# Optimization experiments

Hardware: AMD Instinct MI355X
Metric: run time of the kernel (lower is better)

Reference implementation:

```python
import jax, jax.numpy as jnp
import numpy as np

N = 50000   # num_nodes
T = 24      # window_size
H = 64      # hidden_dim
HOR = 12    # horizon
E = 1600000 # num edges


def setup_inputs() -> dict:
    key = jax.random.key(0)
    ks = jax.random.split(key, 12)
    s = 1.0 / np.sqrt(H)
    u = lambda k, shape: jax.random.uniform(k, shape, jnp.float32, -s, s)
    return {
        "x": jax.random.normal(ks[0], (N, T), jnp.float32),
        "edge_index": jax.random.randint(ks[1], (2, E), 0, N, dtype=jnp.int32),
        "w_ih": u(ks[2], (3 * H, 1)),
        "w_hh": u(ks[3], (3 * H, H)),
        "b_ih": u(ks[4], (3 * H,)),
        "b_hh": u(ks[5], (3 * H,)),
        "gc1_w": u(ks[6], (H, H)),
        "gc1_b": u(ks[7], (H,)),
        "gc2_w": u(ks[8], (H, H)),
        "gc2_b": u(ks[9], (H,)),
        "fc_w": u(ks[10], (HOR, H)),
        "fc_b": u(ks[11], (HOR,)),
    }


def _gru_last(x, w_ih, w_hh, b_ih, b_hh):
    # x: [N, T] scalar-per-step input (input_size=1). Returns final hidden [N, H].
    h0 = jnp.zeros((x.shape[0], H), x.dtype)

    def step(h, xt):  # xt: [N]
        gi = xt[:, None] * w_ih[:, 0][None, :] + b_ih   # [N, 3H]
        gh = h @ w_hh.T + b_hh                          # [N, 3H]
        i_r, i_z, i_n = jnp.split(gi, 3, axis=-1)
        h_r, h_z, h_n = jnp.split(gh, 3, axis=-1)
        r = jax.nn.sigmoid(i_r + h_r)
        z = jax.nn.sigmoid(i_z + h_z)
        n = jnp.tanh(i_n + r * h_n)
        h = (1.0 - z) * n + z * h
        return h, None

    hT, _ = jax.lax.scan(step, h0, x.T)  # scan over time axis
    return hT


def _gcn_norm(edge_index, n):
    # PyG GCNConv: add self loops, symmetric D^-1/2 (A+I) D^-1/2 normalization.
    loops = jnp.arange(n, dtype=edge_index.dtype)
    src = jnp.concatenate([edge_index[0], loops])
    dst = jnp.concatenate([edge_index[1], loops])
    deg = jax.ops.segment_sum(jnp.ones(src.shape, jnp.float32), dst, num_segments=n)
    dinv = jnp.where(deg > 0, jax.lax.rsqrt(jnp.maximum(deg, 1e-12)), 0.0)
    return src, dst, dinv[src] * dinv[dst]


def _gcn(h, src, dst, norm, W, b, n):
    hw = h @ W.T                      # [N, H] linear transform first
    msg = hw[src] * norm[:, None]     # gather + edge weighting
    return jax.ops.segment_sum(msg, dst, num_segments=n) + b


def reference(x, edge_index, w_ih, w_hh, b_ih, b_hh, gc1_w, gc1_b, gc2_w, gc2_b, fc_w, fc_b):
    n = x.shape[0]
    h = _gru_last(x, w_ih, w_hh, b_ih, b_hh)            # [N, H] last GRU output
    src, dst, norm = _gcn_norm(edge_index, n)
    h = jax.nn.relu(_gcn(h, src, dst, norm, gc1_w, gc1_b, n))
    h = jax.nn.relu(_gcn(h, src, dst, norm, gc2_w, gc2_b, n))
    return h @ fc_w.T + fc_b                            # [N, HOR]
```

## Files before the change

kernel.cpp:

```cpp
#include <hip/hip_runtime.h>

#define NN 50000
#define TT 24
#define HH 64
#define HORZ 12
#define EE 1600000

#define GP 256
#define EP (EE / GP)
#define BK 784
#define NBG (BK * GP)
#define SCB (NBG / 512)
#define BKA ((NN + 63) / 64)

typedef __attribute__((ext_vector_type(8))) _Float16 f16x8;
typedef __attribute__((ext_vector_type(4))) _Float16 f16x4;
typedef __attribute__((ext_vector_type(4))) float f32x4;

__device__ __forceinline__ float sigm(float x) {
  return __builtin_amdgcn_rcpf(1.f + __expf(-x));
}
__device__ __forceinline__ float tanh_f(float x) {
  return 1.f - 2.f * __builtin_amdgcn_rcpf(1.f + __expf(2.f * x));
}

__global__ __launch_bounds__(256) void p1_frags_kernel(
    const int* __restrict__ dst, int* __restrict__ hist,
    const float* __restrict__ whh, const float* __restrict__ g1,
    const float* __restrict__ g2, const float* __restrict__ fcw,
    _Float16* __restrict__ frag) {
  int bid = blockIdx.x;
  if (bid >= GP) {
    int idx = (bid - GP) * 256 + threadIdx.x;
    if (idx >= 21504) return;
    const float* W;
    int rows, li;
    if (idx < 12288) { W = whh; rows = 192; li = idx; }
    else if (idx < 16384) { W = g1; rows = 64; li = idx - 12288; }
    else if (idx < 20480) { W = g2; rows = 64; li = idx - 16384; }
    else { W = fcw; rows = HORZ; li = idx - 20480; }
    int j = li & 7;
    int l = (li >> 3) & 63;
    int kf = (li >> 9) & 1;
    int nf = li >> 10;
    int col = 16 * nf + (l & 15);
    int k = 32 * kf + 8 * (l >> 4) + j;
    frag[idx] = (col < rows) ? (_Float16)W[col * 64 + k] : (_Float16)0.f;
    return;
  }
  __shared__ int h[BK];
  int tid = threadIdx.x, g = bid;
  for (int b = tid; b < BK; b += 256) h[b] = 0;
  __syncthreads();
  int e0 = g * EP;
  for (int i = tid; i < EP; i += 256) atomicAdd(&h[dst[e0 + i] >> 6], 1);
  __syncthreads();
  for (int b = tid; b < BK; b += 256) hist[b * GP + g] = h[b];
}

__global__ void scanA_kernel(const int* __restrict__ v, int* __restrict__ part) {
  __shared__ int s[512];
  int i = blockIdx.x * 512 + threadIdx.x;
  s[threadIdx.x] = v[i];
  __syncthreads();
  for (int off = 256; off > 0; off >>= 1) {
    if (threadIdx.x < off) s[threadIdx.x] += s[threadIdx.x + off];
    __syncthreads();
  }
  if (threadIdx.x == 0) part[blockIdx.x] = s[0];
}

__global__ void scanB_kernel(int* __restrict__ part) {
  __shared__ int s[512];
  int t = threadIdx.x;
  int v = (t < SCB) ? part[t] : 0;
  s[t] = v;
  __syncthreads();
  for (int off = 1; off < 512; off <<= 1) {
    int a = s[t];
    int b = (t >= off) ? s[t - off] : 0;
    __syncthreads();
    s[t] = a + b;
    __syncthreads();
  }
  if (t < SCB) part[t] = s[t] - v;
}

__global__ void scanC_kernel(int* __restrict__ cellbase, const int* __restrict__ part) {
  __shared__ int s[2][512];
  int tid = threadIdx.x;
  int i = blockIdx.x * 512 + tid;
  int x = cellbase[i];
  s[0][tid] = x;
  __syncthreads();
  int cur = 0;
  for (int off = 1; off < 512; off <<= 1) {
    int nxt = cur ^ 1;
    int val = s[cur][tid] + ((tid >= off) ? s[cur][tid - off] : 0);
    s[nxt][tid] = val;
    __syncthreads();
    cur = nxt;
  }
  cellbase[i] = part[blockIdx.x] + s[cur][tid] - x;
  if (i == 0) cellbase[NBG] = EE;
}

__global__ __launch_bounds__(256) void p2_scatter_kernel(
    const int* __restrict__ src, const int* __restrict__ dst,
    const int* __restrict__ cellbase, unsigned int* __restrict__ rec) {
  __shared__ int cur[BK];
  int tid = threadIdx.x, g = blockIdx.x;
  for (int b = tid; b < BK; b += 256) cur[b] = cellbase[b * GP + g];
  __syncthreads();
  int e0 = g * EP;
  for (int i = tid; i < EP; i += 256) {
    int e = e0 + i;
    int d = dst[e];
    int s = src[e];
    int p = atomicAdd(&cur[d >> 6], 1);
    rec[p] = ((unsigned)(d & 63) << 16) | (unsigned)s;
  }
}

__global__ __launch_bounds__(256) void sort2_kernel(
    const unsigned int* __restrict__ rec, const int* __restrict__ cellbase,
    unsigned short* __restrict__ csr, int* __restrict__ row_start,
    float* __restrict__ dinv) {
  __shared__ int cnt[64];
  __shared__ int cur[64];
  int b = blockIdx.x, tid = threadIdx.x;
  if (tid < 64) cnt[tid] = 0;
  __syncthreads();
  int e0 = cellbase[b * GP], e1 = cellbase[(b + 1) * GP];
  for (int e = e0 + tid; e < e1; e += 256) atomicAdd(&cnt[rec[e] >> 16], 1);
  __syncthreads();
  if (tid == 0) {
    int a = e0;
#pragma unroll
    for (int l = 0; l < 64; ++l) { int c = cnt[l]; cur[l] = a; a += c; }
  }
  __syncthreads();
  if (tid < 64) {
    int n = b * 64 + tid;
    if (n <= NN) row_start[n] = cur[tid];
    if (n < NN) dinv[n] = rsqrtf((float)(cnt[tid] + 1));
  }
  __syncthreads();
  for (int e = e0 + tid; e < e1; e += 256) {
    unsigned int r = rec[e];
    int p = atomicAdd(&cur[r >> 16], 1);
    csr[p] = (unsigned short)(r & 0xFFFFu);
  }
}

__global__ __launch_bounds__(256, 5) void gru_kernel(
    const float* __restrict__ x, const float* __restrict__ w_ih,
    const float* __restrict__ b_ih, const float* __restrict__ b_hh,
    const _Float16* __restrict__ wfrag, const _Float16* __restrict__ l1f,
    const float* __restrict__ dinv, _Float16* __restrict__ hw) {
  __shared__ __align__(16) _Float16 sh[2][16][72];
  __shared__ __align__(16) float xs[TT][16];

  const int tid = threadIdx.x;
  const int lane = tid & 63;
  const int w = tid >> 6;
  const int c = lane & 15;
  const int q = lane >> 4;

  f16x8 Ar0 = *(const f16x8*)&wfrag[(((w)*2 + 0) * 64 + lane) * 8];
  f16x8 Ar1 = *(const f16x8*)&wfrag[(((w)*2 + 1) * 64 + lane) * 8];
  f16x8 Az0 = *(const f16x8*)&wfrag[(((4 + w) * 2 + 0) * 64 + lane) * 8];
  f16x8 Az1 = *(const f16x8*)&wfrag[(((4 + w) * 2 + 1) * 64 + lane) * 8];
  f16x8 An0 = *(const f16x8*)&wfrag[(((8 + w) * 2 + 0) * 64 + lane) * 8];
  f16x8 An1 = *(const f16x8*)&wfrag[(((8 + w) * 2 + 1) * 64 + lane) * 8];

  float wir[4], wiz[4], win[4], arb[4], azb[4], binc[4], bhnc[4];
#pragma unroll
  for (int r = 0; r < 4; ++r) {
    int dd = 16 * w + 4 * q + r;
    wir[r] = w_ih[dd]; wiz[r] = w_ih[64 + dd]; win[r] = w_ih[128 + dd];
    arb[r] = b_ih[dd] + b_hh[dd];
    azb[r] = b_ih[64 + dd] + b_hh[64 + dd];
    binc[r] = b_ih[128 + dd];
    bhnc[r] = b_hh[128 + dd];
  }

  const int base = blockIdx.x * 16;

  for (int i = tid; i < 16 * TT; i += 256) {
    int nl = i / TT;
    int t = i - nl * TT;
    xs[t][nl] = x[(base + nl) * TT + t];
  }
  __syncthreads();

  float hreg[4] = {0.f, 0.f, 0.f, 0.f};

#pragma unroll 1
  for (int tp = 0; tp < TT / 2; ++tp) {
#pragma unroll
    for (int half = 0; half < 2; ++half) {
      const int t = 2 * tp + half;
      f32x4 ar = (f32x4){arb[0], arb[1], arb[2], arb[3]};
      f32x4 az = (f32x4){azb[0], azb[1], azb[2], azb[3]};
      f32x4 an = (f32x4){bhnc[0], bhnc[1], bhnc[2], bhnc[3]};
      if (t > 0) {
        const _Float16* S = &sh[half ^ 1][0][0];
        f16x8 b0 = *(const f16x8*)&S[c * 72 + 8 * q];
        f16x8 b1 = *(const f16x8*)&S[c * 72 + 32 + 8 * q];
        ar = __builtin_amdgcn_mfma_f32_16x16x32_f16(Ar0, b0, ar, 0, 0, 0);
        az = __builtin_amdgcn_mfma_f32_16x16x32_f16(Az0, b0, az, 0, 0, 0);
        an = __builtin_amdgcn_mfma_f32_16x16x32_f16(An0, b0, an, 0, 0, 0);
        ar = __builtin_amdgcn_mfma_f32_16x16x32_f16(Ar1, b1, ar, 0, 0, 0);
        az = __builtin_amdgcn_mfma_f32_16x16x32_f16(Az1, b1, az, 0, 0, 0);
        an = __builtin_amdgcn_mfma_f32_16x16x32_f16(An1, b1, an, 0, 0, 0);
      }
      float xv = xs[t][c];
      f16x4 hpack;
#pragma unroll
      for (int r = 0; r < 4; ++r) {
        float rg = sigm(xv * wir[r] + ar[r]);
        float zg = sigm(xv * wiz[r] + az[r]);
        float nn = tanh_f(rg * an[r] + (xv * win[r] + binc[r]));
        float hn = nn + zg * (hreg[r] - nn);
        hreg[r] = hn;
        hpack[r] = (_Float16)hn;
      }
      *(f16x4*)&sh[half][c][16 * w + 4 * q] = hpack;
      __syncthreads();
    }
  }

  {
    f16x8 L0 = *(const f16x8*)&l1f[((w * 2 + 0) * 64 + lane) * 8];
    f16x8 L1 = *(const f16x8*)&l1f[((w * 2 + 1) * 64 + lane) * 8];
    const _Float16* S = &sh[1][0][0];
    f16x8 b0 = *(const f16x8*)&S[c * 72 + 8 * q];
    f16x8 b1 = *(const f16x8*)&S[c * 72 + 32 + 8 * q];
    f32x4 acc = (f32x4){0.f, 0.f, 0.f, 0.f};
    acc = __builtin_amdgcn_mfma_f32_16x16x32_f16(L0, b0, acc, 0, 0, 0);
    acc = __builtin_amdgcn_mfma_f32_16x16x32_f16(L1, b1, acc, 0, 0, 0);
    float dn = dinv[base + c];
    f16x4 opack;
#pragma unroll
    for (int r = 0; r < 4; ++r) opack[r] = (_Float16)(acc[r] * dn);
    *(f16x4*)&hw[(base + c) * 64 + 16 * w + 4 * q] = opack;
  }
}

__global__ __launch_bounds__(1024, 4) void agg_lin_kernel(
    const _Float16* __restrict__ hwp, const float* __restrict__ dinv,
    const int* __restrict__ row_start, const unsigned short* __restrict__ csr,
    const float* __restrict__ bias, const _Float16* __restrict__ l2f,
    _Float16* __restrict__ out) {
  __shared__ __align__(16) _Float16 h1[64][72];
  int tid = threadIdx.x, b = blockIdx.x;
  int wv = tid >> 6, lane = tid & 63;
  float bl = bias[lane];
#pragma unroll 1
  for (int k = 0; k < 4; ++k) {
    int row = wv * 4 + k;
    int n = b * 64 + row;
    float v = 0.f;
    if (n < NN) {
      int e0 = row_start[n], e1 = row_start[n + 1];
      float a0 = (float)hwp[n * 64 + lane];
      float a1 = 0.f, a2 = 0.f, a3 = 0.f;
      int e = e0;
      for (; e < e1 && (e & 7); ++e) a0 += (float)hwp[(int)csr[e] * 64 + lane];
      for (; e + 16 <= e1; e += 16) {
        uint4 p0 = *(const uint4*)&csr[e];
        uint4 p1 = *(const uint4*)&csr[e + 8];
        a0 += (float)hwp[(p0.x & 0xFFFF) * 64 + lane];
        a1 += (float)hwp[(p0.x >> 16) * 64 + lane];
        a2 += (float)hwp[(p0.y & 0xFFFF) * 64 + lane];
        a3 += (float)hwp[(p0.y >> 16) * 64 + lane];
        a0 += (float)hwp[(p0.z & 0xFFFF) * 64 + lane];
        a1 += (float)hwp[(p0.z >> 16) * 64 + lane];
        a2 += (float)hwp[(p0.w & 0xFFFF) * 64 + lane];
        a3 += (float)hwp[(p0.w >> 16) * 64 + lane];
        a0 += (float)hwp[(p1.x & 0xFFFF) * 64 + lane];
        a1 += (float)hwp[(p1.x >> 16) * 64 + lane];
        a2 += (float)hwp[(p1.y & 0xFFFF) * 64 + lane];
        a3 += (float)hwp[(p1.y >> 16) * 64 + lane];
        a0 += (float)hwp[(p1.z & 0xFFFF) * 64 + lane];
        a1 += (float)hwp[(p1.z >> 16) * 64 + lane];
        a2 += (float)hwp[(p1.w & 0xFFFF) * 64 + lane];
        a3 += (float)hwp[(p1.w >> 16) * 64 + lane];
      }
      for (; e + 8 <= e1; e += 8) {
        uint4 pk = *(const uint4*)&csr[e];
        a0 += (float)hwp[(pk.x & 0xFFFF) * 64 + lane];
        a1 += (float)hwp[(pk.x >> 16) * 64 + lane];
        a2 += (float)hwp[(pk.y & 0xFFFF) * 64 + lane];
        a3 += (float)hwp[(pk.y >> 16) * 64 + lane];
        a0 += (float)hwp[(pk.z & 0xFFFF) * 64 + lane];
        a1 += (float)hwp[(pk.z >> 16) * 64 + lane];
        a2 += (float)hwp[(pk.w & 0xFFFF) * 64 + lane];
        a3 += (float)hwp[(pk.w >> 16) * 64 + lane];
      }
      for (; e < e1; ++e) a0 += (float)hwp[(int)csr[e] * 64 + lane];
      v = (a0 + a1 + a2 + a3) * dinv[n] + bl;
      v = v > 0.f ? v : 0.f;
    }
    h1[row][lane] = (_Float16)v;
  }
  __syncthreads();
  int g = wv >> 2, wq = wv & 3;
  int c = lane & 15, q = lane >> 4;
  f16x8 B0 = *(const f16x8*)&l2f[((wq * 2 + 0) * 64 + lane) * 8];
  f16x8 B1 = *(const f16x8*)&l2f[((wq * 2 + 1) * 64 + lane) * 8];
  f16x8 a0 = *(const f16x8*)&h1[16 * g + c][8 * q];
  f16x8 a1 = *(const f16x8*)&h1[16 * g + c][32 + 8 * q];
  f32x4 acc = (f32x4){0.f, 0.f, 0.f, 0.f};
  acc = __builtin_amdgcn_mfma_f32_16x16x32_f16(a0, B0, acc, 0, 0, 0);
  acc = __builtin_amdgcn_mfma_f32_16x16x32_f16(a1, B1, acc, 0, 0, 0);
#pragma unroll
  for (int r = 0; r < 4; ++r) {
    int n = b * 64 + 16 * g + 4 * q + r;
    if (n < NN) out[n * 64 + 16 * wq + c] = (_Float16)(acc[r] * dinv[n]);
  }
}

__global__ __launch_bounds__(1024, 4) void agg_fc_kernel(
    const _Float16* __restrict__ hwp, const float* __restrict__ dinv,
    const int* __restrict__ row_start, const unsigned short* __restrict__ csr,
    const float* __restrict__ bias, const _Float16* __restrict__ fcf,
    const float* __restrict__ fcb, float* __restrict__ out) {
  __shared__ __align__(16) _Float16 h1[64][72];
  int tid = threadIdx.x, b = blockIdx.x;
  int wv = tid >> 6, lane = tid & 63;
  float bl = bias[lane];
#pragma unroll 1
  for (int k = 0; k < 4; ++k) {
    int row = wv * 4 + k;
    int n = b * 64 + row;
    float v = 0.f;
    if (n < NN) {
      int e0 = row_start[n], e1 = row_start[n + 1];
      float a0 = (float)hwp[n * 64 + lane];
      float a1 = 0.f, a2 = 0.f, a3 = 0.f;
      int e = e0;
      for (; e < e1 && (e & 7); ++e) a0 += (float)hwp[(int)csr[e] * 64 + lane];
      for (; e + 16 <= e1; e += 16) {
        uint4 p0 = *(const uint4*)&csr[e];
        uint4 p1 = *(const uint4*)&csr[e + 8];
        a0 += (float)hwp[(p0.x & 0xFFFF) * 64 + lane];
        a1 += (float)hwp[(p0.x >> 16) * 64 + lane];
        a2 += (float)hwp[(p0.y & 0xFFFF) * 64 + lane];
        a3 += (float)hwp[(p0.y >> 16) * 64 + lane];
        a0 += (float)hwp[(p0.z & 0xFFFF) * 64 + lane];
        a1 += (float)hwp[(p0.z >> 16) * 64 + lane];
        a2 += (float)hwp[(p0.w & 0xFFFF) * 64 + lane];
        a3 += (float)hwp[(p0.w >> 16) * 64 + lane];
        a0 += (float)hwp[(p1.x & 0xFFFF) * 64 + lane];
        a1 += (float)hwp[(p1.x >> 16) * 64 + lane];
        a2 += (float)hwp[(p1.y & 0xFFFF) * 64 + lane];
        a3 += (float)hwp[(p1.y >> 16) * 64 + lane];
        a0 += (float)hwp[(p1.z & 0xFFFF) * 64 + lane];
        a1 += (float)hwp[(p1.z >> 16) * 64 + lane];
        a2 += (float)hwp[(p1.w & 0xFFFF) * 64 + lane];
        a3 += (float)hwp[(p1.w >> 16) * 64 + lane];
      }
      for (; e + 8 <= e1; e += 8) {
        uint4 pk = *(const uint4*)&csr[e];
        a0 += (float)hwp[(pk.x & 0xFFFF) * 64 + lane];
        a1 += (float)hwp[(pk.x >> 16) * 64 + lane];
        a2 += (float)hwp[(pk.y & 0xFFFF) * 64 + lane];
        a3 += (float)hwp[(pk.y >> 16) * 64 + lane];
        a0 += (float)hwp[(pk.z & 0xFFFF) * 64 + lane];
        a1 += (float)hwp[(pk.z >> 16) * 64 + lane];
        a2 += (float)hwp[(pk.w & 0xFFFF) * 64 + lane];
        a3 += (float)hwp[(pk.w >> 16) * 64 + lane];
      }
      for (; e < e1; ++e) a0 += (float)hwp[(int)csr[e] * 64 + lane];
      v = (a0 + a1 + a2 + a3) * dinv[n] + bl;
      v = v > 0.f ? v : 0.f;
    }
    h1[row][lane] = (_Float16)v;
  }
  __syncthreads();
  if (wv < 4) {
    int g = wv;
    int c = lane & 15, q = lane >> 4;
    f16x8 B0 = *(const f16x8*)&fcf[(0 * 64 + lane) * 8];
    f16x8 B1 = *(const f16x8*)&fcf[(1 * 64 + lane) * 8];
    f16x8 a0 = *(const f16x8*)&h1[16 * g + c][8 * q];
    f16x8 a1 = *(const f16x8*)&h1[16 * g + c][32 + 8 * q];
    float bc = (c < HORZ) ? fcb[c] : 0.f;
    f32x4 acc = (f32x4){bc, bc, bc, bc};
    acc = __builtin_amdgcn_mfma_f32_16x16x32_f16(a0, B0, acc, 0, 0, 0);
    acc = __builtin_amdgcn_mfma_f32_16x16x32_f16(a1, B1, acc, 0, 0, 0);
    if (c < HORZ) {
#pragma unroll
      for (int r = 0; r < 4; ++r) {
        int n = b * 64 + 16 * g + 4 * q + r;
        if (n < NN) out[n * HORZ + c] = acc[r];
      }
    }
  }
}

extern "C" void kernel_launch(void* const* d_in, const int* in_sizes, int n_in,
                              void* d_out, int out_size, void* d_ws, size_t ws_size,
                              hipStream_t stream) {
  (void)in_sizes; (void)n_in; (void)out_size; (void)ws_size;
  const float* x = (const float*)d_in[0];
  const int* edge_index = (const int*)d_in[1];
  const float* w_ih = (const float*)d_in[2];
  const float* w_hh = (const float*)d_in[3];
  const float* b_ih = (const float*)d_in[4];
  const float* b_hh = (const float*)d_in[5];
  const float* gc1_w = (const float*)d_in[6];
  const float* gc1_b = (const float*)d_in[7];
  const float* gc2_w = (const float*)d_in[8];
  const float* gc2_b = (const float*)d_in[9];
  const float* fc_w = (const float*)d_in[10];
  const float* fc_b = (const float*)d_in[11];
  float* out = (float*)d_out;

  char* ws = (char*)d_ws;
  _Float16* wfrag = (_Float16*)ws;
  _Float16* l1f = wfrag + 12288;
  _Float16* l2f = l1f + 4096;
  _Float16* fcf = l2f + 4096;
  _Float16* hw1 = (_Float16*)(ws + 43008);
  _Float16* hw2 = hw1 + NN * 64;
  float* dinv = (float*)(hw2 + NN * 64);
  int* row_start = (int*)(dinv + NN);
  int* cellbase = row_start + 50240;
  int* part = cellbase + NBG + 4;
  unsigned int* rec = (unsigned int*)(part + 512);
  unsigned short* csr = (unsigned short*)(rec + EE);

  const int* esrc = edge_index;
  const int* edst = edge_index + EE;

  p1_frags_kernel<<<GP + 84, 256, 0, stream>>>(edst, cellbase, w_hh, gc1_w, gc2_w, fc_w, wfrag);
  scanA_kernel<<<SCB, 512, 0, stream>>>(cellbase, part);
  scanB_kernel<<<1, 512, 0, stream>>>(part);
  scanC_kernel<<<SCB, 512, 0, stream>>>(cellbase, part);
  p2_scatter_kernel<<<GP, 256, 0, stream>>>(esrc, edst, cellbase, rec);
  sort2_kernel<<<BK, 256, 0, stream>>>(rec, cellbase, csr, row_start, dinv);

  gru_kernel<<<NN / 16, 256, 0, stream>>>(x, w_ih, b_ih, b_hh, wfrag, l1f, dinv, hw1);
  agg_lin_kernel<<<BKA, 1024, 0, stream>>>(hw1, dinv, row_start, csr, gc1_b, l2f, hw2);
  agg_fc_kernel<<<BKA, 1024, 0, stream>>>(hw2, dinv, row_start, csr, gc2_b, fcf, fc_b, out);
}
```

Before: 240.8 us.

## Give each GRU wave its own 16-node tile and fold input/bias into MFMA

The GRU kernel now gives each wave an independent 16-node tile and computes all 64 hidden units for it, so 64 nodes go to a block and the per-timestep block-wide __syncthreads is removed. The input term x*w_ih and the biases are folded into an extra MFMA against a fragment that holds x and 1, and the log2(e) scaling is baked into the fp16 weights so exp2f can be used. In exchange the kernel holds many more weight fragments in registers (launch bounds drop to 2), does more MFMA work per wave, and rounds the biases and input weights to fp16.

```diff
diff --git a/kernel.cpp b/kernel.cpp
--- a/kernel.cpp
+++ b/kernel.cpp
@@ -13,39 +13,66 @@
 #define SCB (NBG / 512)
 #define BKA ((NN + 63) / 64)
 
+#define L2E 1.44269504088896340736f
+#define NFRAG_GRU 24576
+#define NFRAG_ALL 33792
+
 typedef __attribute__((ext_vector_type(8))) _Float16 f16x8;
 typedef __attribute__((ext_vector_type(4))) _Float16 f16x4;
 typedef __attribute__((ext_vector_type(4))) float f32x4;
 
-__device__ __forceinline__ float sigm(float x) {
-  return __builtin_amdgcn_rcpf(1.f + __expf(-x));
-}
-__device__ __forceinline__ float tanh_f(float x) {
-  return 1.f - 2.f * __builtin_amdgcn_rcpf(1.f + __expf(2.f * x));
-}
-
 __global__ __launch_bounds__(256) void p1_frags_kernel(
     const int* __restrict__ dst, int* __restrict__ hist,
-    const float* __restrict__ whh, const float* __restrict__ g1,
-    const float* __restrict__ g2, const float* __restrict__ fcw,
-    _Float16* __restrict__ frag) {
+    const float* __restrict__ whh, const float* __restrict__ wih,
+    const float* __restrict__ bih, const float* __restrict__ bhh,
+    const float* __restrict__ g1, const float* __restrict__ g2,
+    const float* __restrict__ fcw, _Float16* __restrict__ frag) {
   int bid = blockIdx.x;
   if (bid >= GP) {
     int idx = (bid - GP) * 256 + threadIdx.x;
-    if (idx >= 21504) return;
-    const float* W;
-    int rows, li;
-    if (idx < 12288) { W = whh; rows = 192; li = idx; }
-    else if (idx < 16384) { W = g1; rows = 64; li = idx - 12288; }
-    else if (idx < 20480) { W = g2; rows = 64; li = idx - 16384; }
-    else { W = fcw; rows = HORZ; li = idx - 20480; }
-    int j = li & 7;
-    int l = (li >> 3) & 63;
-    int kf = (li >> 9) & 1;
-    int nf = li >> 10;
-    int col = 16 * nf + (l & 15);
-    int k = 32 * kf + 8 * (l >> 4) + j;
-    frag[idx] = (col < rows) ? (_Float16)W[col * 64 + k] : (_Float16)0.f;
+    if (idx >= NFRAG_ALL) return;
+    float v = 0.f;
+    if (idx < NFRAG_GRU) {
+      int tl = idx / 1536;
+      int rem = idx - tl * 1536;
+      int kf = rem >> 9;
+      int l = (rem >> 3) & 63;
+      int j = rem & 7;
+      int rit = l & 15;
+      int half = l >> 4;
+      if (tl < 12) {
+        int g = tl >> 2, dq = tl & 3;
+        int row = g * 64 + 16 * dq + rit;
+        float sc = (g == 2) ? 2.f * L2E : L2E;
+        if (kf < 2) {
+          v = whh[row * 64 + 32 * kf + 8 * half + j] * sc;
+        } else {
+          int kl = 8 * half + j;
+          if (kl == 0) v = (tl < 8) ? wih[row] * sc : 0.f;
+          else if (kl == 1) v = (tl < 8) ? (bih[row] + bhh[row]) * sc : bhh[row] * sc;
+        }
+      } else if (kf == 2) {
+        int row = 128 + 16 * (tl - 12) + rit;
+        int kl = 8 * half + j;
+        if (kl == 0) v = wih[row] * 2.f * L2E;
+        else if (kl == 1) v = bih[row] * 2.f * L2E;
+      }
+    } else {
+      int li = idx - NFRAG_GRU;
+      const float* W;
+      int rows;
+      if (li < 4096) { W = g1; rows = 64; }
+      else if (li < 8192) { W = g2; rows = 64; li -= 4096; }
+      else { W = fcw; rows = HORZ; li -= 8192; }
+      int j = li & 7;
+      int l = (li >> 3) & 63;
+      int kf = (li >> 9) & 1;
+      int nf = li >> 10;
+      int col = 16 * nf + (l & 15);
+      int k = 32 * kf + 8 * (l >> 4) + j;
+      v = (col < rows) ? W[col * 64 + k] : 0.f;
+    }
+    frag[idx] = (_Float16)v;
     return;
   }
   __shared__ int h[BK];
@@ -153,13 +180,12 @@
   }
 }
 
-__global__ __launch_bounds__(256, 5) void gru_kernel(
-    const float* __restrict__ x, const float* __restrict__ w_ih,
-    const float* __restrict__ b_ih, const float* __restrict__ b_hh,
-    const _Float16* __restrict__ wfrag, const _Float16* __restrict__ l1f,
-    const float* __restrict__ dinv, _Float16* __restrict__ hw) {
-  __shared__ __align__(16) _Float16 sh[2][16][72];
-  __shared__ __align__(16) float xs[TT][16];
+__global__ __launch_bounds__(256, 2) void gru_kernel(
+    const float* __restrict__ x, const _Float16* __restrict__ gf,
+    const _Float16* __restrict__ l1f, const float* __restrict__ dinv,
+    _Float16* __restrict__ hw) {
+  __shared__ __align__(16) _Float16 sh[4][2][16][72];
+  __shared__ __align__(16) float xs[TT][64];
 
   const int tid = threadIdx.x;
   const int lane = tid & 63;
@@ -167,84 +193,97 @@
   const int c = lane & 15;
   const int q = lane >> 4;
 
-  f16x8 Ar0 = *(const f16x8*)&wfrag[(((w)*2 + 0) * 64 + lane) * 8];
-  f16x8 Ar1 = *(const f16x8*)&wfrag[(((w)*2 + 1) * 64 + lane) * 8];
-  f16x8 Az0 = *(const f16x8*)&wfrag[(((4 + w) * 2 + 0) * 64 + lane) * 8];
-  f16x8 Az1 = *(const f16x8*)&wfrag[(((4 + w) * 2 + 1) * 64 + lane) * 8];
-  f16x8 An0 = *(const f16x8*)&wfrag[(((8 + w) * 2 + 0) * 64 + lane) * 8];
-  f16x8 An1 = *(const f16x8*)&wfrag[(((8 + w) * 2 + 1) * 64 + lane) * 8];
-
-  float wir[4], wiz[4], win[4], arb[4], azb[4], binc[4], bhnc[4];
-#pragma unroll
-  for (int r = 0; r < 4; ++r) {
-    int dd = 16 * w + 4 * q + r;
-    wir[r] = w_ih[dd]; wiz[r] = w_ih[64 + dd]; win[r] = w_ih[128 + dd];
-    arb[r] = b_ih[dd] + b_hh[dd];
-    azb[r] = b_ih[64 + dd] + b_hh[64 + dd];
-    binc[r] = b_ih[128 + dd];
-    bhnc[r] = b_hh[128 + dd];
-  }
-
-  const int base = blockIdx.x * 16;
-
-  for (int i = tid; i < 16 * TT; i += 256) {
+  f16x8 A0[12], A1[12], A2[16];
+#pragma unroll
+  for (int tl = 0; tl < 12; ++tl) {
+    A0[tl] = *(const f16x8*)&gf[((tl * 3 + 0) * 64 + lane) * 8];
+    A1[tl] = *(const f16x8*)&gf[((tl * 3 + 1) * 64 + lane) * 8];
+  }
+#pragma unroll
+  for (int tl = 0; tl < 16; ++tl)
+    A2[tl] = *(const f16x8*)&gf[((tl * 3 + 2) * 64 + lane) * 8];
+
+  const int nb = blockIdx.x * 64;
+  for (int i = tid; i < 64 * TT; i += 256) {
     int nl = i / TT;
     int t = i - nl * TT;
-    xs[t][nl] = x[(base + nl) * TT + t];
-  }
-  __syncthreads();
-
-  float hreg[4] = {0.f, 0.f, 0.f, 0.f};
+    int node = nb + nl;
+    if (node >= NN) node = NN - 1;
+    xs[t][nl] = x[node * TT + t];
+  }
+  {
+    f16x4 z4 = {(_Float16)0.f, (_Float16)0.f, (_Float16)0.f, (_Float16)0.f};
+#pragma unroll
+    for (int dq = 0; dq < 4; ++dq)
+      *(f16x4*)&sh[w][1][c][16 * dq + 4 * q] = z4;
+  }
+  __syncthreads();
+
+  const f32x4 zero4 = (f32x4){0.f, 0.f, 0.f, 0.f};
+  float hreg[4][4];
+#pragma unroll
+  for (int dq = 0; dq < 4; ++dq)
+#pragma unroll
+    for (int r = 0; r < 4; ++r) hreg[dq][r] = 0.f;
+
+  f16x8 b2 = {(_Float16)0.f, (_Float16)0.f, (_Float16)0.f, (_Float16)0.f,
+              (_Float16)0.f, (_Float16)0.f, (_Float16)0.f, (_Float16)0.f};
+  b2[1] = (q == 0) ? (_Float16)1.f : (_Float16)0.f;
 
 #pragma unroll 1
-  for (int tp = 0; tp < TT / 2; ++tp) {
-#pragma unroll
-    for (int half = 0; half < 2; ++half) {
-      const int t = 2 * tp + half;
-      f32x4 ar = (f32x4){arb[0], arb[1], arb[2], arb[3]};
-      f32x4 az = (f32x4){azb[0], azb[1], azb[2], azb[3]};
-      f32x4 an = (f32x4){bhnc[0], bhnc[1], bhnc[2], bhnc[3]};
-      if (t > 0) {
-        const _Float16* S = &sh[half ^ 1][0][0];
-        f16x8 b0 = *(const f16x8*)&S[c * 72 + 8 * q];
-        f16x8 b1 = *(const f16x8*)&S[c * 72 + 32 + 8 * q];
-        ar = __builtin_amdgcn_mfma_f32_16x16x32_f16(Ar0, b0, ar, 0, 0, 0);
-        az = __builtin_amdgcn_mfma_f32_16x16x32_f16(Az0, b0, az, 0, 0, 0);
-        an = __builtin_amdgcn_mfma_f32_16x16x32_f16(An0, b0, an, 0, 0, 0);
-        ar = __builtin_amdgcn_mfma_f32_16x16x32_f16(Ar1, b1, ar, 0, 0, 0);
-        az = __builtin_amdgcn_mfma_f32_16x16x32_f16(Az1, b1, az, 0, 0, 0);
-        an = __builtin_amdgcn_mfma_f32_16x16x32_f16(An1, b1, an, 0, 0, 0);
-      }
-      float xv = xs[t][c];
-      f16x4 hpack;
-#pragma unroll
-      for (int r = 0; r < 4; ++r) {
-        float rg = sigm(xv * wir[r] + ar[r]);
-        float zg = sigm(xv * wiz[r] + az[r]);
-        float nn = tanh_f(rg * an[r] + (xv * win[r] + binc[r]));
-        float hn = nn + zg * (hreg[r] - nn);
-        hreg[r] = hn;
-        hpack[r] = (_Float16)hn;
-      }
-      *(f16x4*)&sh[half][c][16 * w + 4 * q] = hpack;
-      __syncthreads();
-    }
-  }
-
-  {
-    f16x8 L0 = *(const f16x8*)&l1f[((w * 2 + 0) * 64 + lane) * 8];
-    f16x8 L1 = *(const f16x8*)&l1f[((w * 2 + 1) * 64 + lane) * 8];
-    const _Float16* S = &sh[1][0][0];
+  for (int t = 0; t < TT; ++t) {
+    const int buf = t & 1;
+    const _Float16* S = &sh[w][buf ^ 1][0][0];
     f16x8 b0 = *(const f16x8*)&S[c * 72 + 8 * q];
     f16x8 b1 = *(const f16x8*)&S[c * 72 + 32 + 8 * q];
-    f32x4 acc = (f32x4){0.f, 0.f, 0.f, 0.f};
-    acc = __builtin_amdgcn_mfma_f32_16x16x32_f16(L0, b0, acc, 0, 0, 0);
-    acc = __builtin_amdgcn_mfma_f32_16x16x32_f16(L1, b1, acc, 0, 0, 0);
-    float dn = dinv[base + c];
-    f16x4 opack;
-#pragma unroll
-    for (int r = 0; r < 4; ++r) opack[r] = (_Float16)(acc[r] * dn);
-    *(f16x4*)&hw[(base + c) * 64 + 16 * w + 4 * q] = opack;
+    float xv = xs[t][w * 16 + c];
+    b2[0] = (q == 0) ? (_Float16)xv : (_Float16)0.f;
+#pragma unroll
+    for (int dq = 0; dq < 4; ++dq) {
+      f32x4 ar = __builtin_amdgcn_mfma_f32_16x16x32_f16(A2[dq], b2, zero4, 0, 0, 0);
+      ar = __builtin_amdgcn_mfma_f32_16x16x32_f16(A0[dq], b0, ar, 0, 0, 0);
+      ar = __builtin_amdgcn_mfma_f32_16x16x32_f16(A1[dq], b1, ar, 0, 0, 0);
+      f32x4 az = __builtin_amdgcn_mfma_f32_16x16x32_f16(A2[4 + dq], b2, zero4, 0, 0, 0);
+      az = __builtin_amdgcn_mfma_f32_16x16x32_f16(A0[4 + dq], b0, az, 0, 0, 0);
+      az = __builtin_amdgcn_mfma_f32_16x16x32_f16(A1[4 + dq], b1, az, 0, 0, 0);
+      f32x4 aa = __builtin_amdgcn_mfma_f32_16x16x32_f16(A2[8 + dq], b2, zero4, 0, 0, 0);
+      aa = __builtin_amdgcn_mfma_f32_16x16x32_f16(A0[8 + dq], b0, aa, 0, 0, 0);
+      aa = __builtin_amdgcn_mfma_f32_16x16x32_f16(A1[8 + dq], b1, aa, 0, 0, 0);
+      f32x4 ax = __builtin_amdgcn_mfma_f32_16x16x32_f16(A2[12 + dq], b2, zero4, 0, 0, 0);
+      f16x4 hp;
+#pragma unroll
+      for (int r = 0; r < 4; ++r) {
+        float rg = __builtin_amdgcn_rcpf(1.f + exp2f(-ar[r]));
+        float zg = __builtin_amdgcn_rcpf(1.f + exp2f(-az[r]));
+        float tt = __builtin_amdgcn_rcpf(1.f + exp2f(fmaf(rg, aa[r], ax[r])));
+        float nn = fmaf(-2.f, tt, 1.f);
+        float hn = nn + zg * (hreg[dq][r] - nn);
+        hreg[dq][r] = hn;
+        hp[r] = (_Float16)hn;
+      }
+      *(f16x4*)&sh[w][buf][c][16 * dq + 4 * q] = hp;
+    }
+  }
+
+  {
+    const _Float16* S = &sh[w][1][0][0];
+    f16x8 e0 = *(const f16x8*)&S[c * 72 + 8 * q];
+    f16x8 e1 = *(const f16x8*)&S[c * 72 + 32 + 8 * q];
+    int n = nb + w * 16 + c;
+    if (n < NN) {
+      float dn = dinv[n];
+#pragma unroll
+      for (int dq = 0; dq < 4; ++dq) {
+        f16x8 L0 = *(const f16x8*)&l1f[((dq * 2 + 0) * 64 + lane) * 8];
+        f16x8 L1 = *(const f16x8*)&l1f[((dq * 2 + 1) * 64 + lane) * 8];
+        f32x4 a = __builtin_amdgcn_mfma_f32_16x16x32_f16(L0, e0, zero4, 0, 0, 0);
+        a = __builtin_amdgcn_mfma_f32_16x16x32_f16(L1, e1, a, 0, 0, 0);
+        f16x4 op;
+#pragma unroll
+        for (int r = 0; r < 4; ++r) op[r] = (_Float16)(a[r] * dn);
+        *(f16x4*)&hw[n * 64 + 16 * dq + 4 * q] = op;
+      }
+    }
   }
 }
 
@@ -420,11 +459,11 @@
   float* out = (float*)d_out;
 
   char* ws = (char*)d_ws;
-  _Float16* wfrag = (_Float16*)ws;
-  _Float16* l1f = wfrag + 12288;
+  _Float16* gf = (_Float16*)ws;
+  _Float16* l1f = gf + NFRAG_GRU;
   _Float16* l2f = l1f + 4096;
   _Float16* fcf = l2f + 4096;
-  _Float16* hw1 = (_Float16*)(ws + 43008);
+  _Float16* hw1 = (_Float16*)(ws + 67584);
   _Float16* hw2 = hw1 + NN * 64;
   float* dinv = (float*)(hw2 + NN * 64);
   int* row_start = (int*)(dinv + NN);
@@ -436,14 +475,15 @@
   const int* esrc = edge_index;
   const int* edst = edge_index + EE;
 
-  p1_frags_kernel<<<GP + 84, 256, 0, stream>>>(edst, cellbase, w_hh, gc1_w, gc2_w, fc_w, wfrag);
+  p1_frags_kernel<<<GP + 132, 256, 0, stream>>>(edst, cellbase, w_hh, w_ih, b_ih,
+                                                b_hh, gc1_w, gc2_w, fc_w, gf);
   scanA_kernel<<<SCB, 512, 0, stream>>>(cellbase, part);
   scanB_kernel<<<1, 512, 0, stream>>>(part);
   scanC_kernel<<<SCB, 512, 0, stream>>>(cellbase, part);
   p2_scatter_kernel<<<GP, 256, 0, stream>>>(esrc, edst, cellbase, rec);
   sort2_kernel<<<BK, 256, 0, stream>>>(rec, cellbase, csr, row_start, dinv);
 
-  gru_kernel<<<NN / 16, 256, 0, stream>>>(x, w_ih, b_ih, b_hh, wfrag, l1f, dinv, hw1);
+  gru_kernel<<<(NN + 63) / 64, 256, 0, stream>>>(x, gf, l1f, dinv, hw1);
   agg_lin_kernel<<<BKA, 1024, 0, stream>>>(hw1, dinv, row_start, csr, gc1_b, l2f, hw2);
   agg_fc_kernel<<<BKA, 1024, 0, stream>>>(hw2, dinv, row_start, csr, gc2_b, fcf, fc_b, out);
 }
```

After: 280.6 us. 1.17x slower.
